# Performance work log

Hardware: AMD Instinct MI355X
Metric: run time of the kernel (lower is better)

The kernel has to match this reference:

```python
import jax, jax.numpy as jnp
import numpy as np

N_NODES = 100000
N_EDGES = 1600000
HIDDEN = 64
LEAKY_SLOPE = 0.01  # torch F.leaky_relu default


def setup_inputs() -> dict:
    key = jax.random.key(0)
    k1, k2, k3, k4 = jax.random.split(key, 4)
    x = jax.random.normal(k1, (N_NODES, HIDDEN), dtype=jnp.float32)
    edge_index = jax.random.randint(k2, (2, N_EDGES), 0, N_NODES, dtype=jnp.int64)
    # Linear(hidden, 1, bias=False) weights, squeezed to [hidden]
    w_i = jax.random.normal(k3, (HIDDEN,), dtype=jnp.float32) * 0.1
    w_j = jax.random.normal(k4, (HIDDEN,), dtype=jnp.float32) * 0.1
    return {"x": x, "edge_index": edge_index, "w_i": w_i, "w_j": w_j}


def reference(x, edge_index, w_i, w_j):
    n = x.shape[0]
    ej, ei = edge_index[0], edge_index[1]  # (edge_index_j, edge_index_i)
    # per-node attention scores, then per-edge gather
    s_i = x @ w_i  # [N]
    s_j = x @ w_j  # [N]
    e = jax.nn.leaky_relu(s_i[ei] + s_j[ej], LEAKY_SLOPE)  # [E]
    # segment softmax over edges grouped by destination node ei
    emax = jax.ops.segment_max(e, ei, num_segments=n)  # [N]
    ex = jnp.exp(e - emax[ei])  # [E]
    denom = jax.ops.segment_sum(ex, ei, num_segments=n)  # [N]
    alpha = ex / denom[ei]  # [E]
    # spmm: out[i] = sum_{edges e: dst=i} alpha_e * x[src_e]
    out = jax.ops.segment_sum(alpha[:, None] * x[ej], ei, num_segments=n)  # [N, H]
    return jax.nn.relu(out)
```

## Files before the change

kernel.cpp:

```cpp
#include <hip/hip_runtime.h>
#include <stdint.h>

#define N_NODES 100000
#define N_EDGES 1600000
#define HIDDEN  64
#define SLOPE   0.01f
#define NBUCK   782
#define CAPB    2816
#define PCHUNK  4096
#define NPART   391
#define NSB     25000
#define NCAP    48

__device__ __forceinline__ unsigned short f2bf(float f) {
    uint32_t u = __float_as_uint(f);
    uint32_t r = u + 0x7FFFu + ((u >> 16) & 1u);
    return (unsigned short)(r >> 16);
}

__global__ void __launch_bounds__(256) k_build(const float* __restrict__ x,
                                               const float* __restrict__ w_i,
                                               const float* __restrict__ w_j,
                                               const int* __restrict__ srcs,
                                               const int* __restrict__ dsts,
                                               float* __restrict__ s_i,
                                               float* __restrict__ s_j,
                                               unsigned short* __restrict__ xb,
                                               int* __restrict__ cursor,
                                               uint32_t* __restrict__ pairs) {
    __shared__ int lcnt[NBUCK], lbase[NBUCK];
    int tid = threadIdx.x;
    if (blockIdx.x >= NPART) {
        int node = (blockIdx.x - NPART) * 4 + (tid >> 6);
        int lane = tid & 63;
        if (node >= N_NODES) return;
        float v = x[node * HIDDEN + lane];
        xb[node * HIDDEN + lane] = f2bf(v);
        float a = v * w_i[lane];
        float b = v * w_j[lane];
        for (int off = 32; off > 0; off >>= 1) {
            a += __shfl_xor(a, off, 64);
            b += __shfl_xor(b, off, 64);
        }
        if (lane == 0) { s_i[node] = a; s_j[node] = b; }
        return;
    }
    for (int b = tid; b < NBUCK; b += 256) lcnt[b] = 0;
    __syncthreads();
    int e0 = blockIdx.x * PCHUNK;
    int e1 = min(e0 + PCHUNK, N_EDGES);
    for (int e = e0 + tid; e < e1; e += 256)
        atomicAdd(&lcnt[dsts[e] >> 7], 1);
    __syncthreads();
    for (int b = tid; b < NBUCK; b += 256) {
        int c = lcnt[b];
        lbase[b] = c ? atomicAdd(&cursor[b], c) : 0;
        lcnt[b] = 0;
    }
    __syncthreads();
    for (int e = e0 + tid; e < e1; e += 256) {
        int src = srcs[e];
        int dst = dsts[e];
        int b = dst >> 7;
        int r = atomicAdd(&lcnt[b], 1);
        int pos = lbase[b] + r;
        if (pos < CAPB)
            pairs[(size_t)b * CAPB + pos] =
                ((uint32_t)(dst & 127) << 24) | (uint32_t)src;
    }
}

__device__ __forceinline__ float bflo(uint32_t d) { return __uint_as_float(d << 16); }
__device__ __forceinline__ float bfhi(uint32_t d) { return __uint_as_float(d & 0xFFFF0000u); }

template <int L>
__device__ __forceinline__ void gat_batch4(const uint64_t* pp, int i, int quarter, int ql,
                                           const uint2* __restrict__ xw2,
                                           float acc[4], float& den) {
    uint64_t q[L];
    uint2 d[L];
#pragma unroll
    for (int t = 0; t < L; ++t) q[t] = pp[i + 4 * t + quarter];
#pragma unroll
    for (int t = 0; t < L; ++t)
        d[t] = xw2[((uint32_t)q[t] & 0xFFFFFFu) * 16 + ql];
#pragma unroll
    for (int t = 0; t < L; ++t) {
        float w = __uint_as_float((uint32_t)(q[t] >> 32));
        den += w;
        acc[0] = fmaf(w, bflo(d[t].x), acc[0]);
        acc[1] = fmaf(w, bfhi(d[t].x), acc[1]);
        acc[2] = fmaf(w, bflo(d[t].y), acc[2]);
        acc[3] = fmaf(w, bfhi(d[t].y), acc[3]);
    }
}

__global__ void __launch_bounds__(256, 8) k_bucket_agg(const uint2* __restrict__ xw2,
                                                       const uint32_t* __restrict__ pairs,
                                                       const int* __restrict__ cursor,
                                                       const float* __restrict__ s_i,
                                                       const float* __restrict__ s_j,
                                                       float* __restrict__ out) {
    __shared__ uint64_t spairs[32 * NCAP];
    __shared__ int lcur[32];
    __shared__ float s_si[32];
    int tid = threadIdx.x;
    int g = blockIdx.x;
    int cb = g >> 2, sub = g & 3;
    int node0 = g * 32;
    const uint32_t* reg = pairs + (size_t)cb * CAPB;
    int rcnt = min(cursor[cb], CAPB);
    if (tid < 32) {
        lcur[tid] = 0;
        int node = node0 + tid;
        s_si[tid] = (node < N_NODES) ? s_i[node] : 0.f;
    }
    __syncthreads();
    for (int e = tid; e < rcnt; e += 256) {
        uint32_t p = reg[e];
        int dstl = (int)(p >> 24);
        if ((dstl >> 5) == sub) {
            int n = dstl & 31;
            int src = (int)(p & 0xFFFFFFu);
            float sc = s_si[n] + s_j[src];
            sc = (sc > 0.f) ? sc : SLOPE * sc;
            float w = __expf(sc);
            int slot = atomicAdd(&lcur[n], 1);
            if (slot < NCAP)
                spairs[n * NCAP + slot] =
                    ((uint64_t)__float_as_uint(w) << 32) | (uint32_t)src;
        }
    }
    __syncthreads();
    int wave = tid >> 6, lane = tid & 63;
    int quarter = lane >> 4, ql = lane & 15;
    for (int k = wave; k < 32; k += 4) {
        int node = node0 + k;
        if (node >= N_NODES) break;
        float acc[4] = {0.f, 0.f, 0.f, 0.f};
        float den = 0.f;
        int c = lcur[k];
        if (c <= NCAP) {
            const uint64_t* pp = spairs + k * NCAP;
            int i = 0;
            for (; i + 16 <= c; i += 16) gat_batch4<4>(pp, i, quarter, ql, xw2, acc, den);
            if (i + 8 <= c) { gat_batch4<2>(pp, i, quarter, ql, xw2, acc, den); i += 8; }
            if (i + 4 <= c) { gat_batch4<1>(pp, i, quarter, ql, xw2, acc, den); i += 4; }
            int rem = c - i;
            if (rem > 0) {
                uint64_t q = pp[i + min(quarter, rem - 1)];
                float w = (quarter < rem) ? __uint_as_float((uint32_t)(q >> 32)) : 0.f;
                uint2 d = xw2[((uint32_t)q & 0xFFFFFFu) * 16 + ql];
                den += w;
                acc[0] = fmaf(w, bflo(d.x), acc[0]);
                acc[1] = fmaf(w, bfhi(d.x), acc[1]);
                acc[2] = fmaf(w, bflo(d.y), acc[2]);
                acc[3] = fmaf(w, bfhi(d.y), acc[3]);
            }
        } else {
            int sn = (sub << 5) | k;
            for (int e = 0; e < rcnt; ++e) {
                uint32_t p = reg[e];
                if ((int)(p >> 24) == sn) {
                    int src = (int)(p & 0xFFFFFFu);
                    float sc = s_si[k] + s_j[src];
                    sc = (sc > 0.f) ? sc : SLOPE * sc;
                    float w = (quarter == 0) ? __expf(sc) : 0.f;
                    uint2 d = xw2[(uint32_t)src * 16 + ql];
                    den += w;
                    acc[0] = fmaf(w, bflo(d.x), acc[0]);
                    acc[1] = fmaf(w, bfhi(d.x), acc[1]);
                    acc[2] = fmaf(w, bflo(d.y), acc[2]);
                    acc[3] = fmaf(w, bfhi(d.y), acc[3]);
                }
            }
        }
#pragma unroll
        for (int j = 0; j < 4; ++j) {
            acc[j] += __shfl_xor(acc[j], 16, 64);
            acc[j] += __shfl_xor(acc[j], 32, 64);
        }
        den += __shfl_xor(den, 16, 64);
        den += __shfl_xor(den, 32, 64);
        if (quarter == 0) {
            float4 r = make_float4(0.f, 0.f, 0.f, 0.f);
            if (c > 0) {
                float inv = 1.f / den;
                r.x = fmaxf(acc[0] * inv, 0.f);
                r.y = fmaxf(acc[1] * inv, 0.f);
                r.z = fmaxf(acc[2] * inv, 0.f);
                r.w = fmaxf(acc[3] * inv, 0.f);
            }
            ((float4*)(out + (size_t)node * HIDDEN))[ql] = r;
        }
    }
}

extern "C" void kernel_launch(void* const* d_in, const int* in_sizes, int n_in,
                              void* d_out, int out_size, void* d_ws, size_t ws_size,
                              hipStream_t stream) {
    const float* x   = (const float*)d_in[0];
    const int*   ei  = (const int*)d_in[1];
    const float* w_i = (const float*)d_in[2];
    const float* w_j = (const float*)d_in[3];
    float* out = (float*)d_out;

    char* p = (char*)d_ws;
    float*          s_i    = (float*)p;          p += (size_t)N_NODES * 4;
    float*          s_j    = (float*)p;          p += (size_t)N_NODES * 4;
    unsigned short* xb     = (unsigned short*)p; p += (size_t)N_NODES * HIDDEN * 2;
    int*            cursor = (int*)p;            p += 4096;
    uint32_t*       pairs  = (uint32_t*)p;

    const int* srcs = ei;
    const int* dsts = ei + N_EDGES;

    hipMemsetAsync(cursor, 0, NBUCK * sizeof(int), stream);
    k_build     <<<NPART + NSB, 256, 0, stream>>>(x, w_i, w_j, srcs, dsts,
                                                  s_i, s_j, xb, cursor, pairs);
    k_bucket_agg<<<(N_NODES + 31) / 32, 256, 0, stream>>>((const uint2*)xb, pairs, cursor,
                                                          s_i, s_j, out);
}
```

Baseline: 159.9 us.

## Fuse memset, build and aggregation into one persistent cooperative kernel

Replaces the memset and the two separate kernels with a single cooperative persistent kernel. Block 0 zeroes the bucket cursors and raises a ready flag; partition blocks spin on that flag before reserving bucket slots, while the other blocks compute the scores and the bf16 copy of x. After a grid-wide sync, blocks pull aggregation tiles dynamically through an atomic work counter. This removes launch and memset overhead and balances the aggregation work, but it adds grid-sync and spin-wait cost and caps concurrency at co-resident blocks. The ready flag is never cleared between calls, so on repeated calls the partition blocks may not wait for the reset, which makes correctness fragile.

```diff
diff --git a/kernel.cpp b/kernel.cpp
--- a/kernel.cpp
+++ b/kernel.cpp
@@ -1,5 +1,8 @@
 #include <hip/hip_runtime.h>
+#include <hip/hip_cooperative_groups.h>
 #include <stdint.h>
+
+namespace cg = cooperative_groups;
 
 #define N_NODES 100000
 #define N_EDGES 1600000
@@ -9,65 +12,15 @@
 #define CAPB    2816
 #define PCHUNK  4096
 #define NPART   391
-#define NSB     25000
+#define NSU     25000
+#define NAGG    3125
 #define NCAP    48
+
 
 __device__ __forceinline__ unsigned short f2bf(float f) {
     uint32_t u = __float_as_uint(f);
     uint32_t r = u + 0x7FFFu + ((u >> 16) & 1u);
     return (unsigned short)(r >> 16);
-}
-
-__global__ void __launch_bounds__(256) k_build(const float* __restrict__ x,
-                                               const float* __restrict__ w_i,
-                                               const float* __restrict__ w_j,
-                                               const int* __restrict__ srcs,
-                                               const int* __restrict__ dsts,
-                                               float* __restrict__ s_i,
-                                               float* __restrict__ s_j,
-                                               unsigned short* __restrict__ xb,
-                                               int* __restrict__ cursor,
-                                               uint32_t* __restrict__ pairs) {
-    __shared__ int lcnt[NBUCK], lbase[NBUCK];
-    int tid = threadIdx.x;
-    if (blockIdx.x >= NPART) {
-        int node = (blockIdx.x - NPART) * 4 + (tid >> 6);
-        int lane = tid & 63;
-        if (node >= N_NODES) return;
-        float v = x[node * HIDDEN + lane];
-        xb[node * HIDDEN + lane] = f2bf(v);
-        float a = v * w_i[lane];
-        float b = v * w_j[lane];
-        for (int off = 32; off > 0; off >>= 1) {
-            a += __shfl_xor(a, off, 64);
-            b += __shfl_xor(b, off, 64);
-        }
-        if (lane == 0) { s_i[node] = a; s_j[node] = b; }
-        return;
-    }
-    for (int b = tid; b < NBUCK; b += 256) lcnt[b] = 0;
-    __syncthreads();
-    int e0 = blockIdx.x * PCHUNK;
-    int e1 = min(e0 + PCHUNK, N_EDGES);
-    for (int e = e0 + tid; e < e1; e += 256)
-        atomicAdd(&lcnt[dsts[e] >> 7], 1);
-    __syncthreads();
-    for (int b = tid; b < NBUCK; b += 256) {
-        int c = lcnt[b];
-        lbase[b] = c ? atomicAdd(&cursor[b], c) : 0;
-        lcnt[b] = 0;
-    }
-    __syncthreads();
-    for (int e = e0 + tid; e < e1; e += 256) {
-        int src = srcs[e];
-        int dst = dsts[e];
-        int b = dst >> 7;
-        int r = atomicAdd(&lcnt[b], 1);
-        int pos = lbase[b] + r;
-        if (pos < CAPB)
-            pairs[(size_t)b * CAPB + pos] =
-                ((uint32_t)(dst & 127) << 24) | (uint32_t)src;
-    }
 }
 
 __device__ __forceinline__ float bflo(uint32_t d) { return __uint_as_float(d << 16); }
@@ -95,104 +48,177 @@
     }
 }
 
-__global__ void __launch_bounds__(256, 8) k_bucket_agg(const uint2* __restrict__ xw2,
-                                                       const uint32_t* __restrict__ pairs,
-                                                       const int* __restrict__ cursor,
-                                                       const float* __restrict__ s_i,
-                                                       const float* __restrict__ s_j,
-                                                       float* __restrict__ out) {
+__global__ void __launch_bounds__(256, 8)
+k_gat(const float* __restrict__ x,
+      const float* __restrict__ w_i,
+      const float* __restrict__ w_j,
+      const int* __restrict__ srcs,
+      const int* __restrict__ dsts,
+      float* __restrict__ s_i,
+      float* __restrict__ s_j,
+      unsigned short* __restrict__ xb,
+      int* __restrict__ ctrl,
+      uint32_t* __restrict__ pairs,
+      float* __restrict__ out) {
+    __shared__ int lcnt[NBUCK], lbase[NBUCK];
     __shared__ uint64_t spairs[32 * NCAP];
     __shared__ int lcur[32];
     __shared__ float s_si[32];
+    __shared__ int snext;
     int tid = threadIdx.x;
-    int g = blockIdx.x;
-    int cb = g >> 2, sub = g & 3;
-    int node0 = g * 32;
-    const uint32_t* reg = pairs + (size_t)cb * CAPB;
-    int rcnt = min(cursor[cb], CAPB);
-    if (tid < 32) {
-        lcur[tid] = 0;
-        int node = node0 + tid;
-        s_si[tid] = (node < N_NODES) ? s_i[node] : 0.f;
-    }
-    __syncthreads();
-    for (int e = tid; e < rcnt; e += 256) {
-        uint32_t p = reg[e];
-        int dstl = (int)(p >> 24);
-        if ((dstl >> 5) == sub) {
-            int n = dstl & 31;
-            int src = (int)(p & 0xFFFFFFu);
-            float sc = s_si[n] + s_j[src];
-            sc = (sc > 0.f) ? sc : SLOPE * sc;
-            float w = __expf(sc);
-            int slot = atomicAdd(&lcur[n], 1);
-            if (slot < NCAP)
-                spairs[n * NCAP + slot] =
-                    ((uint64_t)__float_as_uint(w) << 32) | (uint32_t)src;
-        }
-    }
-    __syncthreads();
+    int nb  = gridDim.x;
+
+    if (blockIdx.x == 0) {
+        for (int i = tid; i < NBUCK; i += 256) atomicExch(&ctrl[i], 0);
+        __syncthreads();
+        if (tid == 0) {
+            atomicExch(&ctrl[NBUCK + 1], nb);
+            __threadfence();
+            atomicExch(&ctrl[NBUCK], 1);
+        }
+    }
+
+    if (blockIdx.x < NPART) {
+        for (int b = tid; b < NBUCK; b += 256) lcnt[b] = 0;
+        __syncthreads();
+        int e0 = blockIdx.x * PCHUNK;
+        int e1 = min(e0 + PCHUNK, N_EDGES);
+        for (int e = e0 + tid; e < e1; e += 256)
+            atomicAdd(&lcnt[dsts[e] >> 7], 1);
+        if (tid == 0)
+            while (atomicAdd(&ctrl[NBUCK], 0) != 1) {}
+        __syncthreads();
+        for (int b = tid; b < NBUCK; b += 256) {
+            int c = lcnt[b];
+            lbase[b] = c ? atomicAdd(&ctrl[b], c) : 0;
+            lcnt[b] = 0;
+        }
+        __syncthreads();
+        for (int e = e0 + tid; e < e1; e += 256) {
+            int src = srcs[e];
+            int dst = dsts[e];
+            int b = dst >> 7;
+            int r = atomicAdd(&lcnt[b], 1);
+            int pos = lbase[b] + r;
+            if (pos < CAPB)
+                pairs[(size_t)b * CAPB + pos] =
+                    ((uint32_t)(dst & 127) << 24) | (uint32_t)src;
+        }
+    } else {
+        int lane = tid & 63;
+        for (int u = blockIdx.x - NPART; u < NSU; u += nb - NPART) {
+            int node = u * 4 + (tid >> 6);
+            if (node < N_NODES) {
+                float v = x[node * HIDDEN + lane];
+                xb[node * HIDDEN + lane] = f2bf(v);
+                float a = v * w_i[lane];
+                float b = v * w_j[lane];
+                for (int off = 32; off > 0; off >>= 1) {
+                    a += __shfl_xor(a, off, 64);
+                    b += __shfl_xor(b, off, 64);
+                }
+                if (lane == 0) { s_i[node] = a; s_j[node] = b; }
+            }
+        }
+    }
+
+    __threadfence();
+    cg::this_grid().sync();
+
+    const uint2* xw2 = (const uint2*)xb;
     int wave = tid >> 6, lane = tid & 63;
     int quarter = lane >> 4, ql = lane & 15;
-    for (int k = wave; k < 32; k += 4) {
-        int node = node0 + k;
-        if (node >= N_NODES) break;
-        float acc[4] = {0.f, 0.f, 0.f, 0.f};
-        float den = 0.f;
-        int c = lcur[k];
-        if (c <= NCAP) {
-            const uint64_t* pp = spairs + k * NCAP;
-            int i = 0;
-            for (; i + 16 <= c; i += 16) gat_batch4<4>(pp, i, quarter, ql, xw2, acc, den);
-            if (i + 8 <= c) { gat_batch4<2>(pp, i, quarter, ql, xw2, acc, den); i += 8; }
-            if (i + 4 <= c) { gat_batch4<1>(pp, i, quarter, ql, xw2, acc, den); i += 4; }
-            int rem = c - i;
-            if (rem > 0) {
-                uint64_t q = pp[i + min(quarter, rem - 1)];
-                float w = (quarter < rem) ? __uint_as_float((uint32_t)(q >> 32)) : 0.f;
-                uint2 d = xw2[((uint32_t)q & 0xFFFFFFu) * 16 + ql];
-                den += w;
-                acc[0] = fmaf(w, bflo(d.x), acc[0]);
-                acc[1] = fmaf(w, bfhi(d.x), acc[1]);
-                acc[2] = fmaf(w, bflo(d.y), acc[2]);
-                acc[3] = fmaf(w, bfhi(d.y), acc[3]);
-            }
-        } else {
-            int sn = (sub << 5) | k;
-            for (int e = 0; e < rcnt; ++e) {
-                uint32_t p = reg[e];
-                if ((int)(p >> 24) == sn) {
-                    int src = (int)(p & 0xFFFFFFu);
-                    float sc = s_si[k] + s_j[src];
-                    sc = (sc > 0.f) ? sc : SLOPE * sc;
-                    float w = (quarter == 0) ? __expf(sc) : 0.f;
-                    uint2 d = xw2[(uint32_t)src * 16 + ql];
+    int vb = blockIdx.x;
+    while (vb < NAGG) {
+        int cb = vb >> 2, sub = vb & 3;
+        int node0 = vb * 32;
+        const uint32_t* reg = pairs + (size_t)cb * CAPB;
+        int rcnt = min(atomicAdd(&ctrl[cb], 0), CAPB);
+        if (tid < 32) {
+            lcur[tid] = 0;
+            int node = node0 + tid;
+            s_si[tid] = (node < N_NODES) ? s_i[node] : 0.f;
+        }
+        __syncthreads();
+        for (int e = tid; e < rcnt; e += 256) {
+            uint32_t p = reg[e];
+            int dstl = (int)(p >> 24);
+            if ((dstl >> 5) == sub) {
+                int n = dstl & 31;
+                int src = (int)(p & 0xFFFFFFu);
+                float sc = s_si[n] + s_j[src];
+                sc = (sc > 0.f) ? sc : SLOPE * sc;
+                float w = __expf(sc);
+                int slot = atomicAdd(&lcur[n], 1);
+                if (slot < NCAP)
+                    spairs[n * NCAP + slot] =
+                        ((uint64_t)__float_as_uint(w) << 32) | (uint32_t)src;
+            }
+        }
+        __syncthreads();
+        for (int k = wave; k < 32; k += 4) {
+            int node = node0 + k;
+            if (node >= N_NODES) break;
+            float acc[4] = {0.f, 0.f, 0.f, 0.f};
+            float den = 0.f;
+            int c = lcur[k];
+            if (c <= NCAP) {
+                const uint64_t* pp = spairs + k * NCAP;
+                int i = 0;
+                for (; i + 16 <= c; i += 16) gat_batch4<4>(pp, i, quarter, ql, xw2, acc, den);
+                if (i + 8 <= c) { gat_batch4<2>(pp, i, quarter, ql, xw2, acc, den); i += 8; }
+                if (i + 4 <= c) { gat_batch4<1>(pp, i, quarter, ql, xw2, acc, den); i += 4; }
+                int rem = c - i;
+                if (rem > 0) {
+                    uint64_t q = pp[i + min(quarter, rem - 1)];
+                    float w = (quarter < rem) ? __uint_as_float((uint32_t)(q >> 32)) : 0.f;
+                    uint2 d = xw2[((uint32_t)q & 0xFFFFFFu) * 16 + ql];
                     den += w;
                     acc[0] = fmaf(w, bflo(d.x), acc[0]);
                     acc[1] = fmaf(w, bfhi(d.x), acc[1]);
                     acc[2] = fmaf(w, bflo(d.y), acc[2]);
                     acc[3] = fmaf(w, bfhi(d.y), acc[3]);
                 }
-            }
-        }
-#pragma unroll
-        for (int j = 0; j < 4; ++j) {
-            acc[j] += __shfl_xor(acc[j], 16, 64);
-            acc[j] += __shfl_xor(acc[j], 32, 64);
-        }
-        den += __shfl_xor(den, 16, 64);
-        den += __shfl_xor(den, 32, 64);
-        if (quarter == 0) {
-            float4 r = make_float4(0.f, 0.f, 0.f, 0.f);
-            if (c > 0) {
-                float inv = 1.f / den;
-                r.x = fmaxf(acc[0] * inv, 0.f);
-                r.y = fmaxf(acc[1] * inv, 0.f);
-                r.z = fmaxf(acc[2] * inv, 0.f);
-                r.w = fmaxf(acc[3] * inv, 0.f);
-            }
-            ((float4*)(out + (size_t)node * HIDDEN))[ql] = r;
-        }
+            } else {
+                int sn = (sub << 5) | k;
+                for (int e = 0; e < rcnt; ++e) {
+                    uint32_t p = reg[e];
+                    if ((int)(p >> 24) == sn) {
+                        int src = (int)(p & 0xFFFFFFu);
+                        float sc = s_si[k] + s_j[src];
+                        sc = (sc > 0.f) ? sc : SLOPE * sc;
+                        float w = (quarter == 0) ? __expf(sc) : 0.f;
+                        uint2 d = xw2[(uint32_t)src * 16 + ql];
+                        den += w;
+                        acc[0] = fmaf(w, bflo(d.x), acc[0]);
+                        acc[1] = fmaf(w, bfhi(d.x), acc[1]);
+                        acc[2] = fmaf(w, bflo(d.y), acc[2]);
+                        acc[3] = fmaf(w, bfhi(d.y), acc[3]);
+                    }
+                }
+            }
+#pragma unroll
+            for (int j = 0; j < 4; ++j) {
+                acc[j] += __shfl_xor(acc[j], 16, 64);
+                acc[j] += __shfl_xor(acc[j], 32, 64);
+            }
+            den += __shfl_xor(den, 16, 64);
+            den += __shfl_xor(den, 32, 64);
+            if (quarter == 0) {
+                float4 r = make_float4(0.f, 0.f, 0.f, 0.f);
+                if (c > 0) {
+                    float inv = 1.f / den;
+                    r.x = fmaxf(acc[0] * inv, 0.f);
+                    r.y = fmaxf(acc[1] * inv, 0.f);
+                    r.z = fmaxf(acc[2] * inv, 0.f);
+                    r.w = fmaxf(acc[3] * inv, 0.f);
+                }
+                ((float4*)(out + (size_t)node * HIDDEN))[ql] = r;
+            }
+        }
+        if (tid == 0) snext = atomicAdd(&ctrl[NBUCK + 1], 1);
+        __syncthreads();
+        vb = snext;
     }
 }
 
@@ -206,18 +232,24 @@
     float* out = (float*)d_out;
 
     char* p = (char*)d_ws;
-    float*          s_i    = (float*)p;          p += (size_t)N_NODES * 4;
-    float*          s_j    = (float*)p;          p += (size_t)N_NODES * 4;
-    unsigned short* xb     = (unsigned short*)p; p += (size_t)N_NODES * HIDDEN * 2;
-    int*            cursor = (int*)p;            p += 4096;
-    uint32_t*       pairs  = (uint32_t*)p;
+    float*          s_i   = (float*)p;          p += (size_t)N_NODES * 4;
+    float*          s_j   = (float*)p;          p += (size_t)N_NODES * 4;
+    unsigned short* xb    = (unsigned short*)p; p += (size_t)N_NODES * HIDDEN * 2;
+    int*            ctrl  = (int*)p;            p += 4096;
+    uint32_t*       pairs = (uint32_t*)p;
 
     const int* srcs = ei;
     const int* dsts = ei + N_EDGES;
 
-    hipMemsetAsync(cursor, 0, NBUCK * sizeof(int), stream);
-    k_build     <<<NPART + NSB, 256, 0, stream>>>(x, w_i, w_j, srcs, dsts,
-                                                  s_i, s_j, xb, cursor, pairs);
-    k_bucket_agg<<<(N_NODES + 31) / 32, 256, 0, stream>>>((const uint2*)xb, pairs, cursor,
-                                                          s_i, s_j, out);
-}
+    int occ = 0;
+    hipOccupancyMaxActiveBlocksPerMultiprocessor(&occ, k_gat, 256, 0);
+    if (occ < 1) occ = 1;
+    int nblocks = occ * 256;
+    if (nblocks > NAGG) nblocks = NAGG;
+
+    void* args[] = {(void*)&x, (void*)&w_i, (void*)&w_j, (void*)&srcs, (void*)&dsts,
+                    (void*)&s_i, (void*)&s_j, (void*)&xb, (void*)&ctrl, (void*)&pairs,
+                    (void*)&out};
+    hipLaunchCooperativeKernel((const void*)k_gat, dim3(nblocks), dim3(256),
+                               args, 0, stream);
+}
```

New measurement: 470.4 us. 2.94x slower.
